# Performance work log

Measured on AMD Instinct MI355X. Metric: run time of the kernel, lower is better.

The kernel has to match this reference:

```python
import jax, jax.numpy as jnp
import numpy as np

EPS = 1e-5
K = 20


def _bn(x, gamma, beta):
    # BatchNorm in training mode: stats over all axes except last (channel)
    axes = tuple(range(x.ndim - 1))
    m = jnp.mean(x, axes, keepdims=True)
    v = jnp.var(x, axes, keepdims=True)
    return gamma * (x - m) * jax.lax.rsqrt(v + EPS) + beta


def _leaky(x):
    return jax.nn.leaky_relu(x, 0.2)


def _edge_conv(x, W, gamma, beta):
    # x: [B, N, C] channel-last. Faithful to source: topk on cdist with
    # torch default largest=True (k FARTHEST points). Squared distance
    # preserves the ordering of euclidean distance.
    sq = jnp.sum(x * x, axis=-1)                                    # [B,N]
    d2 = sq[:, :, None] + sq[:, None, :] - 2.0 * jnp.einsum('bnc,bmc->bnm', x, x)
    idx = jax.lax.top_k(d2, K)[1]                                   # [B,N,K]
    nbr = jax.vmap(lambda xi, ii: xi[ii])(x, idx)                   # [B,N,K,C]
    ctr = jnp.broadcast_to(x[:, :, None, :], nbr.shape)
    feat = jnp.concatenate([nbr - ctr, ctr], axis=-1)               # [B,N,K,2C]
    h = jnp.einsum('bnkc,oc->bnko', feat, W)                        # 1x1 conv
    return jnp.max(_leaky(_bn(h, gamma, beta)), axis=2)             # [B,N,O]


def _plane(x, w1, g1, b1, w2, g2, b2, w3, g3, b3, w4, g4, b4,
           w5, g5, b5, wl1, g6, b6, wl2, bl2, g7, b7):
    xt = jnp.transpose(x, (0, 2, 1))                                # [B,N,3]
    h1 = _edge_conv(xt, w1, g1, b1)                                 # [B,N,64]
    h2 = _edge_conv(h1, w2, g2, b2)                                 # [B,N,64]
    h3 = _edge_conv(h2, w3, g3, b3)                                 # [B,N,128]
    h4 = _edge_conv(h3, w4, g4, b4)                                 # [B,N,256]
    hc = jnp.concatenate([h1, h2, h3, h4], axis=-1)                 # [B,N,512]
    h = _leaky(_bn(jnp.einsum('bnc,oc->bno', hc, w5), g5, b5))      # [B,N,1024]
    pooled = jnp.concatenate([jnp.max(h, axis=1), jnp.mean(h, axis=1)], axis=-1)  # [B,2048]
    h = _leaky(_bn(pooled @ wl1.T, g6, b6))                         # [B,512]
    h = _leaky(_bn(h @ wl2.T + bl2, g7, b7))                        # [B,256]
    return h  # dropout p=0.0 -> identity


def setup_inputs() -> dict:
    key = jax.random.key(0)
    ks = jax.random.split(key, 16)
    B, N = 8, 2048
    f32 = jnp.float32
    d = {
        'x0': jax.random.normal(ks[0], (B, 3, N), f32),
        'x1': jax.random.normal(ks[1], (B, 3, N), f32),
        'x2': jax.random.normal(ks[2], (B, 3, N), f32),
        'w1': jax.random.normal(ks[3], (64, 6), f32) * 0.3,
        'w2': jax.random.normal(ks[4], (64, 128), f32) * 0.08,
        'w3': jax.random.normal(ks[5], (128, 128), f32) * 0.08,
        'w4': jax.random.normal(ks[6], (256, 256), f32) * 0.06,
        'w5': jax.random.normal(ks[7], (1024, 512), f32) * 0.04,
        'wl1': jax.random.normal(ks[8], (512, 2048), f32) * 0.02,
        'wl2': jax.random.normal(ks[9], (256, 512), f32) * 0.04,
        'bl2': jnp.zeros((256,), f32),
        'whead': jax.random.normal(ks[10], (7, 768), f32) * 0.03,
        'bhead': jnp.zeros((7,), f32),
    }
    for name, c in [('1', 64), ('2', 64), ('3', 128), ('4', 256), ('5', 1024),
                    ('6', 512), ('7', 256), ('8', 7)]:
        d['g' + name] = jnp.ones((c,), f32)
        d['b' + name] = jnp.zeros((c,), f32)
    return d


def reference(x0, x1, x2, w1, g1, b1, w2, g2, b2, w3, g3, b3, w4, g4, b4,
              w5, g5, b5, wl1, g6, b6, wl2, bl2, g7, b7, whead, bhead, g8, b8):
    feats = [
        _plane(x, w1, g1, b1, w2, g2, b2, w3, g3, b3, w4, g4, b4,
               w5, g5, b5, wl1, g6, b6, wl2, bl2, g7, b7)
        for x in (x0, x1, x2)
    ]
    h = jnp.concatenate(feats, axis=-1)                             # [B,768]
    # final MLP head: 1x1 conv on [B,768,1] + BN1d + ReLU + squeeze
    out = jnp.einsum('bc,oc->bo', h, whead) + bhead                 # [B,7]
    out = jax.nn.relu(_bn(out, g8, b8))
    return out
```

## Files before the change

kernel.cpp:

```cpp
#include <hip/hip_runtime.h>
#include <hip/hip_bf16.h>
#include <cstdint>
#include <cstddef>

constexpr int NB = 8;
constexpr int NP = 2048;
constexpr int BN = NB * NP;
constexpr int KK = 20;
constexpr float EPSBN = 1e-5f;
constexpr float NEG = -3.402823466e38f;
constexpr int SLOTS = 8;
constexpr int SLOTSM = 32;
constexpr int SLOTSW = 8;

typedef __attribute__((ext_vector_type(8))) short bf16x8;
typedef __attribute__((ext_vector_type(16))) float f32x16;

__device__ __forceinline__ float leaky(float x) { return x > 0.f ? x : 0.2f * x; }

__device__ __forceinline__ void split2(float x, unsigned short& h, unsigned short& l) {
    __hip_bfloat16 hh = __float2bfloat16(x);
    float hf = __bfloat162float(hh);
    __hip_bfloat16 ll = __float2bfloat16(x - hf);
    h = *reinterpret_cast<unsigned short*>(&hh);
    l = *reinterpret_cast<unsigned short*>(&ll);
}

__device__ __forceinline__ float b2f(unsigned short u) {
    __hip_bfloat16 h = *reinterpret_cast<__hip_bfloat16*>(&u);
    return __bfloat162float(h);
}

__device__ __forceinline__ unsigned int f2key(float f) {
    unsigned int u = __float_as_uint(f);
    return u ^ (unsigned int)(((int)u >> 31) | 0x80000000);
}

__global__ void k_transpose(const float* __restrict__ x, float* __restrict__ xt) {
    int i = blockIdx.x * 256 + threadIdx.x;
    if (i >= BN) return;
    int b = i >> 11, n = i & 2047;
    float4 v;
    v.x = x[(b * 3 + 0) * NP + n];
    v.y = x[(b * 3 + 1) * NP + n];
    v.z = x[(b * 3 + 2) * NP + n];
    v.w = 0.f;
    *(float4*)&xt[(size_t)i * 4] = v;
}

template <int CP4>
__global__ void k_sq4(const float4* __restrict__ FT4, float* __restrict__ sq) {
    int i = blockIdx.x * 256 + threadIdx.x;
    if (i >= BN) return;
    float s = 0.f;
#pragma unroll
    for (int cq = 0; cq < CP4; ++cq) {
        float4 f = FT4[(size_t)cq * BN + i];
        s += f.x * f.x + f.y * f.y + f.z * f.z + f.w * f.w;
    }
    sq[i] = s;
}

template <int CP>
__launch_bounds__(512, 4)
__global__ void k_knn2(const float4* __restrict__ FT4, const float* __restrict__ sq,
                       int* __restrict__ gidx) {
    constexpr int R = 8;
    constexpr int CP4 = CP / 4;
    __shared__ unsigned int ds[R][NP];
    int t = threadIdx.x;
    int b = blockIdx.x >> 8;
    int n0 = (blockIdx.x & 255) * R;
    const float4* FTb = FT4 + (size_t)b * NP;
    const float* sqb = sq + (size_t)b * NP;

    float acc[R][4];
#pragma unroll
    for (int r = 0; r < R; ++r)
#pragma unroll
        for (int mi = 0; mi < 4; ++mi) acc[r][mi] = 0.f;

    for (int cq = 0; cq < CP4; ++cq) {
        float4 f[4];
#pragma unroll
        for (int mi = 0; mi < 4; ++mi)
            f[mi] = FTb[(size_t)cq * BN + t + mi * 512];
#pragma unroll
        for (int r = 0; r < R; ++r) {
            float4 cv = FTb[(size_t)cq * BN + n0 + r];
#pragma unroll
            for (int mi = 0; mi < 4; ++mi)
                acc[r][mi] += f[mi].x * cv.x + f[mi].y * cv.y + f[mi].z * cv.z + f[mi].w * cv.w;
        }
    }
#pragma unroll
    for (int mi = 0; mi < 4; ++mi) {
        int m = t + mi * 512;
        float sm = sqb[m];
#pragma unroll
        for (int r = 0; r < R; ++r) ds[r][m] = f2key(sm - 2.f * acc[r][mi]);
    }
    __syncthreads();

    int wave = t >> 6, lane = t & 63;
    unsigned long long below = (1ull << lane) - 1ull;
    {
        int r = wave;
        unsigned int kv[32];
#pragma unroll
        for (int j = 0; j < 32; ++j) kv[j] = ds[r][lane + 64 * j];

        unsigned int T = 0;
#pragma unroll 1
        for (int bit = 31; bit >= 0; --bit) {
            unsigned int tt = T | (1u << bit);
            int c = 0;
#pragma unroll
            for (int j = 0; j < 32; ++j)
                c += (int)__popcll(__ballot(kv[j] >= tt));
            if (c >= KK) T = tt;
        }

        int obase = (b * NP + n0 + r) * KK;
        int base = 0;
#pragma unroll 1
        for (int j = 0; j < 32; ++j) {
            bool pg = kv[j] > T;
            unsigned long long mk = __ballot(pg);
            if (pg) gidx[obase + base + (int)__popcll(mk & below)] = lane + 64 * j;
            base += (int)__popcll(mk);
        }
        int rem = KK - base;
#pragma unroll 1
        for (int j = 0; j < 32; ++j) {
            if (rem <= 0) break;
            bool pe = kv[j] == T;
            unsigned long long mk = __ballot(pe);
            int myp = (int)__popcll(mk & below);
            if (pe && myp < rem) gidx[obase + base + myp] = lane + 64 * j;
            int cnt = (int)__popcll(mk);
            int take = cnt < rem ? cnt : rem;
            base += take; rem -= take;
        }
    }
}

__global__ void k_prepw(const float* __restrict__ W, int O, int Cact, int CP,
                        float* __restrict__ WaT, float* __restrict__ WdT) {
    int i = blockIdx.x * 256 + threadIdx.x;
    if (i >= CP * O) return;
    int c = i / O, o = i % O;
    float wa = (c < Cact) ? W[o * 2 * Cact + c] : 0.f;
    float wb = (c < Cact) ? W[o * 2 * Cact + Cact + c] : 0.f;
    WaT[i] = wa;
    WdT[i] = wb - wa;
}

__global__ void k_prepws2(const float* __restrict__ W, int O, int C,
                          unsigned short* __restrict__ WcH, unsigned short* __restrict__ WcL) {
    int i = blockIdx.x * 256 + threadIdx.x;
    if (i >= 2 * O * C) return;
    int r = i / C, k = i % C;
    float v;
    if (r < O) v = W[r * 2 * C + k];
    else {
        int o = r - O;
        v = W[o * 2 * C + C + k] - W[o * 2 * C + k];
    }
    split2(v, WcH[i], WcL[i]);
}

__global__ void k_splitw5(const float* __restrict__ w5, unsigned short* __restrict__ w5H,
                          unsigned short* __restrict__ w5L) {
    int i = blockIdx.x * 256 + threadIdx.x;
    if (i >= 1024 * 512) return;
    split2(w5[i], w5H[i], w5L[i]);
}

template <int O, int CP>
__launch_bounds__(O)
__global__ void k_conv(const float* __restrict__ F, int ld, const int* __restrict__ gidx,
                       const float* __restrict__ WaT, const float* __restrict__ WdT,
                       float* __restrict__ hmax, float* __restrict__ s1p,
                       float* __restrict__ s2p) {
    constexpr int CP4 = CP / 4;
    __shared__ float nbrT[2][CP][32];
    __shared__ float sctr[2][CP];
    __shared__ int sidx[2][KK];
    int t = threadIdx.x;
    int p0 = blockIdx.x * 2;
    int b = p0 >> 11;
    const float* Fb = F + (size_t)b * NP * ld;

    if (t < 2 * KK) {
        int pt = t / KK, k = t % KK;
        sidx[pt][k] = gidx[(size_t)(p0 + pt) * KK + k];
    }
    for (int e = t; e < 2 * CP; e += O) {
        int pt = e / CP, cc = e % CP;
        int n = (p0 + pt) & 2047;
        sctr[pt][cc] = Fb[(size_t)n * ld + cc];
    }
    __syncthreads();
    for (int e = t; e < 2 * KK * CP4; e += O) {
        int pt = e / (KK * CP4);
        int e2 = e % (KK * CP4);
        int k = e2 / CP4, cq = e2 % CP4;
        float4 f = *(const float4*)&Fb[(size_t)sidx[pt][k] * ld + cq * 4];
        int kp = (k + 4 * (cq & 7)) & 31;
        nbrT[pt][cq * 4 + 0][kp] = f.x;
        nbrT[pt][cq * 4 + 1][kp] = f.y;
        nbrT[pt][cq * 4 + 2][kp] = f.z;
        nbrT[pt][cq * 4 + 3][kp] = f.w;
    }
    __syncthreads();

    int o = t;
    float bacc0 = 0.f, bacc1 = 0.f;
#pragma unroll 4
    for (int c = 0; c < CP; ++c) {
        float w = WdT[c * O + o];
        bacc0 += sctr[0][c] * w;
        bacc1 += sctr[1][c] * w;
    }
    float a0[KK], a1[KK];
#pragma unroll
    for (int k = 0; k < KK; ++k) { a0[k] = 0.f; a1[k] = 0.f; }
#pragma unroll 2
    for (int c = 0; c < CP; ++c) {
        float w = WaT[c * O + o];
        int s = 4 * ((c >> 2) & 7);
#pragma unroll
        for (int kq = 0; kq < KK / 4; ++kq) {
            int kp = (4 * kq + s) & 31;
            float4 f0 = *(const float4*)&nbrT[0][c][kp];
            float4 f1 = *(const float4*)&nbrT[1][c][kp];
            a0[kq * 4 + 0] += w * f0.x; a1[kq * 4 + 0] += w * f1.x;
            a0[kq * 4 + 1] += w * f0.y; a1[kq * 4 + 1] += w * f1.y;
            a0[kq * 4 + 2] += w * f0.z; a1[kq * 4 + 2] += w * f1.z;
            a0[kq * 4 + 3] += w * f0.w; a1[kq * 4 + 3] += w * f1.w;
        }
    }
    float hm0 = NEG, hm1 = NEG, ts1 = 0.f, ts2 = 0.f;
#pragma unroll
    for (int k = 0; k < KK; ++k) {
        float h0 = a0[k] + bacc0;
        float h1 = a1[k] + bacc1;
        hm0 = fmaxf(hm0, h0); hm1 = fmaxf(hm1, h1);
        ts1 += h0 + h1; ts2 += h0 * h0 + h1 * h1;
    }
    hmax[(size_t)p0 * O + o] = hm0;
    hmax[(size_t)(p0 + 1) * O + o] = hm1;
    int slot = blockIdx.x & (SLOTS - 1);
    atomicAdd(&s1p[slot * O + o], ts1);
    atomicAdd(&s2p[slot * O + o], ts2);
}

template <int O, int C, int COFF>
__launch_bounds__(256, 4)
__global__ void k_gemms(const unsigned short* __restrict__ hcH,
                        const unsigned short* __restrict__ hcL,
                        const unsigned short* __restrict__ WdH,
                        const unsigned short* __restrict__ WdL,
                        float* __restrict__ bacc) {
    constexpr int KS = C / 16;
    int tid = threadIdx.x, wave = tid >> 6, lane = tid & 63;
    int row = lane & 31, half = lane >> 5;
    int p0 = blockIdx.x * 128 + wave * 32;
    int ob = blockIdx.y * 64;
    const unsigned short* aH = hcH + (size_t)(p0 + row) * 512 + COFF;
    const unsigned short* aL = hcL + (size_t)(p0 + row) * 512 + COFF;
    f32x16 acc[2];
#pragma unroll
    for (int nt = 0; nt < 2; ++nt)
#pragma unroll
        for (int r = 0; r < 16; ++r) acc[nt][r] = 0.f;

#pragma unroll 2
    for (int ks = 0; ks < KS; ++ks) {
        int k0 = ks * 16 + half * 8;
        bf16x8 avh = *(const bf16x8*)(aH + k0);
        bf16x8 avl = *(const bf16x8*)(aL + k0);
#pragma unroll
        for (int nt = 0; nt < 2; ++nt) {
            int j = ob + nt * 32 + row;
            bf16x8 bvh = *(const bf16x8*)(WdH + (size_t)j * C + k0);
            bf16x8 bvl = *(const bf16x8*)(WdL + (size_t)j * C + k0);
            acc[nt] = __builtin_amdgcn_mfma_f32_32x32x16_bf16(avh, bvh, acc[nt], 0, 0, 0);
            acc[nt] = __builtin_amdgcn_mfma_f32_32x32x16_bf16(avh, bvl, acc[nt], 0, 0, 0);
            acc[nt] = __builtin_amdgcn_mfma_f32_32x32x16_bf16(avl, bvh, acc[nt], 0, 0, 0);
        }
    }
#pragma unroll
    for (int nt = 0; nt < 2; ++nt)
#pragma unroll
        for (int r = 0; r < 16; ++r) {
            int i = (r & 3) + 8 * (r >> 2) + 4 * half;
            bacc[(size_t)(p0 + i) * O + ob + nt * 32 + row] = acc[nt][r];
        }
}

template <int O>
__launch_bounds__(256)
__global__ void k_gmax(const float* __restrict__ Gz, const int* __restrict__ gidx,
                       float* __restrict__ hmax, float* __restrict__ s1p,
                       float* __restrict__ s2p) {
    constexpr int PB = 256 / O;
    constexpr int O2 = 2 * O;
    __shared__ int sidx[PB][KK];
    int t = threadIdx.x;
    int pt = t / O, o = t % O;
    int p0 = blockIdx.x * PB;
    if (t < PB * KK) sidx[t / KK][t % KK] = gidx[(size_t)(p0 + t / KK) * KK + t % KK];
    __syncthreads();

    int p = p0 + pt;
    int b = p >> 11;
    const float* Gb = Gz + (size_t)b * 2048 * O2;
    float bacc = Gz[(size_t)p * O2 + O + o];
    float mx = NEG, ts1 = 0.f, ts2 = 0.f;
#pragma unroll 5
    for (int k = 0; k < KK; ++k) {
        float g = Gb[(size_t)sidx[pt][k] * O2 + o];
        float h = g + bacc;
        mx = fmaxf(mx, g);
        ts1 += h; ts2 += h * h;
    }
    hmax[(size_t)p * O + o] = mx + bacc;
    int slot = blockIdx.x & (SLOTSM - 1);
    atomicAdd(&s1p[slot * O + o], ts1);
    atomicAdd(&s2p[slot * O + o], ts2);
}

__global__ void k_redslots(const float* __restrict__ s1p, const float* __restrict__ s2p,
                           int O, int S, float* __restrict__ s1g, float* __restrict__ s2g) {
    int o = blockIdx.x * 256 + threadIdx.x;
    if (o >= O) return;
    float a = 0.f, c = 0.f;
    for (int s = 0; s < S; ++s) { a += s1p[s * O + o]; c += s2p[s * O + o]; }
    s1g[o] = a; s2g[o] = c;
}

__global__ void k_bnmax(const float* __restrict__ hmax, int O, const float* __restrict__ s1g,
                        const float* __restrict__ s2g, const float* __restrict__ gam,
                        const float* __restrict__ bet, unsigned short* __restrict__ outH,
                        unsigned short* __restrict__ outL, int ostride, int ooff,
                        float inv_cnt) {
    int i = blockIdx.x * 256 + threadIdx.x;
    if (i >= BN * O) return;
    int o = i % O, p = i / O;
    float m = s1g[o] * inv_cnt;
    float v = s2g[o] * inv_cnt - m * m;
    float rs = rsqrtf(v + EPSBN);
    float y = leaky(gam[o] * (hmax[i] - m) * rs + bet[o]);
    size_t oi = (size_t)p * ostride + ooff + o;
    split2(y, outH[oi], outL[oi]);
}

__global__ void k_pack4(const unsigned short* __restrict__ inH,
                        const unsigned short* __restrict__ inL, int coff,
                        float4* __restrict__ out) {
    __shared__ float tile[64][65];
    int tx = threadIdx.x & 63, ty = threadIdx.x >> 6;
    int p0 = blockIdx.x * 64, o0 = blockIdx.y * 64;
    for (int i = ty; i < 64; i += 4) {
        size_t idx = (size_t)(p0 + i) * 512 + coff + o0 + tx;
        tile[i][tx] = b2f(inH[idx]) + b2f(inL[idx]);
    }
    __syncthreads();
    for (int q = ty; q < 16; q += 4) {
        float4 v;
        v.x = tile[tx][4 * q + 0];
        v.y = tile[tx][4 * q + 1];
        v.z = tile[tx][4 * q + 2];
        v.w = tile[tx][4 * q + 3];
        out[(size_t)(o0 / 4 + q) * BN + p0 + tx] = v;
    }
}

__launch_bounds__(256, 3)
__global__ void k_w5ms(const unsigned short* __restrict__ hcH,
                       const unsigned short* __restrict__ hcL,
                       const unsigned short* __restrict__ w5H,
                       const unsigned short* __restrict__ w5L,
                       float* __restrict__ g5, float* __restrict__ s1p,
                       float* __restrict__ s2p) {
    int tid = threadIdx.x, wave = tid >> 6, lane = tid & 63;
    int row = lane & 31, half = lane >> 5;
    int p0 = blockIdx.x * 32;
    int ob = blockIdx.y * 512 + wave * 128;
    const unsigned short* aH = hcH + (size_t)(p0 + row) * 512;
    const unsigned short* aL = hcL + (size_t)(p0 + row) * 512;
    f32x16 acc[4];
#pragma unroll
    for (int nt = 0; nt < 4; ++nt)
#pragma unroll
        for (int r = 0; r < 16; ++r) acc[nt][r] = 0.f;

#pragma unroll 2
    for (int ks = 0; ks < 32; ++ks) {
        int k0 = ks * 16 + half * 8;
        bf16x8 avh = *(const bf16x8*)(aH + k0);
        bf16x8 avl = *(const bf16x8*)(aL + k0);
#pragma unroll
        for (int nt = 0; nt < 4; ++nt) {
            int j = ob + nt * 32 + row;
            bf16x8 bvh = *(const bf16x8*)(w5H + (size_t)j * 512 + k0);
            bf16x8 bvl = *(const bf16x8*)(w5L + (size_t)j * 512 + k0);
            acc[nt] = __builtin_amdgcn_mfma_f32_32x32x16_bf16(avh, bvh, acc[nt], 0, 0, 0);
            acc[nt] = __builtin_amdgcn_mfma_f32_32x32x16_bf16(avh, bvl, acc[nt], 0, 0, 0);
            acc[nt] = __builtin_amdgcn_mfma_f32_32x32x16_bf16(avl, bvh, acc[nt], 0, 0, 0);
        }
    }
    int slot = blockIdx.x & (SLOTSW - 1);
#pragma unroll
    for (int nt = 0; nt < 4; ++nt) {
        int j = ob + nt * 32 + row;
        float s1 = 0.f, s2 = 0.f;
#pragma unroll
        for (int r = 0; r < 16; ++r) {
            int i = (r & 3) + 8 * (r >> 2) + 4 * half;
            float v = acc[nt][r];
            g5[(size_t)(p0 + i) * 1024 + j] = v;
            s1 += v; s2 += v * v;
        }
        s1 += __shfl_xor(s1, 32);
        s2 += __shfl_xor(s2, 32);
        if (half == 0) {
            atomicAdd(&s1p[slot * 1024 + j], s1);
            atomicAdd(&s2p[slot * 1024 + j], s2);
        }
    }
}

__global__ void k_pool(const float* __restrict__ gbuf, const float* __restrict__ s1g,
                       const float* __restrict__ s2g, const float* __restrict__ gam,
                       const float* __restrict__ bet, float* __restrict__ pmax,
                       float* __restrict__ psum) {
    int t = threadIdx.x;
    int blk = blockIdx.x;
    int nc = blk & 7, ot = (blk >> 3) & 3, b = blk >> 5;
    int o = ot * 256 + t;
    float m = s1g[o] * (1.f / 16384.f);
    float v = s2g[o] * (1.f / 16384.f) - m * m;
    float rs = rsqrtf(v + EPSBN);
    float ga = gam[o], be = bet[o];
    float vmax = NEG, vsum = 0.f;
    for (int j = 0; j < 256; ++j) {
        int n = nc * 256 + j;
        float x = gbuf[((size_t)b * NP + n) * 1024 + o];
        float y = leaky(ga * (x - m) * rs + be);
        vmax = fmaxf(vmax, y);
        vsum += y;
    }
    pmax[(b * 1024 + o) * 8 + nc] = vmax;
    psum[(b * 1024 + o) * 8 + nc] = vsum;
}

__global__ void k_poolfin(const float* __restrict__ pmax, const float* __restrict__ psum,
                          float* __restrict__ pooled) {
    int i = blockIdx.x * 256 + threadIdx.x;
    if (i >= 8192) return;
    float mx = NEG, sm = 0.f;
    for (int j = 0; j < 8; ++j) {
        mx = fmaxf(mx, pmax[i * 8 + j]);
        sm += psum[i * 8 + j];
    }
    int b = i >> 10, o = i & 1023;
    pooled[b * 2048 + o] = mx;
    pooled[b * 2048 + 1024 + o] = sm * (1.f / 2048.f);
}

template <int CIN>
__global__ void k_fc(const float* __restrict__ in, const float* __restrict__ W,
                     const float* __restrict__ bias, int O, float* __restrict__ z) {
    int i = blockIdx.x * 256 + threadIdx.x;
    if (i >= NB * O) return;
    int b = i / O, o = i % O;
    const float* wr = W + (size_t)o * CIN;
    const float* ir = in + (size_t)b * CIN;
    float acc = 0.f;
#pragma unroll 4
    for (int cq = 0; cq < CIN / 4; ++cq) {
        float4 wv = *(const float4*)&wr[cq * 4];
        float4 iv = *(const float4*)&ir[cq * 4];
        acc += wv.x * iv.x + wv.y * iv.y + wv.z * iv.z + wv.w * iv.w;
    }
    z[i] = acc + (bias ? bias[o] : 0.f);
}

__global__ void k_bnb(const float* __restrict__ z, int O, const float* __restrict__ gam,
                      const float* __restrict__ bet, float* __restrict__ out, int ostride,
                      int ooff) {
    int o = blockIdx.x * 256 + threadIdx.x;
    if (o >= O) return;
    float s1 = 0.f, s2 = 0.f;
#pragma unroll
    for (int b = 0; b < NB; ++b) {
        float x = z[b * O + o];
        s1 += x; s2 += x * x;
    }
    float m = s1 * 0.125f, v = s2 * 0.125f - m * m;
    float rs = rsqrtf(v + EPSBN);
    float ga = gam[o], be = bet[o];
    for (int b = 0; b < NB; ++b) {
        float y = ga * (z[b * O + o] - m) * rs + be;
        out[b * ostride + ooff + o] = leaky(y);
    }
}

__global__ void k_head(const float* __restrict__ hf, const float* __restrict__ wh,
                       const float* __restrict__ bh, const float* __restrict__ g8,
                       const float* __restrict__ b8, float* __restrict__ out) {
    __shared__ float zh[56];
    int t = threadIdx.x;
    if (t < 56) {
        int b = t / 7, o = t % 7;
        float acc = bh[o];
        for (int c = 0; c < 768; ++c) acc += hf[b * 768 + c] * wh[o * 768 + c];
        zh[t] = acc;
    }
    __syncthreads();
    if (t < 7) {
        float s1 = 0.f, s2 = 0.f;
        for (int b = 0; b < NB; ++b) {
            float x = zh[b * 7 + t];
            s1 += x; s2 += x * x;
        }
        float m = s1 * 0.125f, v = s2 * 0.125f - m * m;
        float rs = rsqrtf(v + EPSBN);
        for (int b = 0; b < NB; ++b) {
            float y = g8[t] * (zh[b * 7 + t] - m) * rs + b8[t];
            out[b * 7 + t] = fmaxf(y, 0.f);
        }
    }
}

extern "C" void kernel_launch(void* const* d_in, const int* in_sizes, int n_in, void* d_out,
                              int out_size, void* d_ws, size_t ws_size, hipStream_t stream) {
    const float* x[3] = {(const float*)d_in[0], (const float*)d_in[1], (const float*)d_in[2]};
    const float* w1 = (const float*)d_in[3];
    const float* w2 = (const float*)d_in[4];
    const float* w3 = (const float*)d_in[5];
    const float* w4 = (const float*)d_in[6];
    const float* w5 = (const float*)d_in[7];
    const float* wl1 = (const float*)d_in[8];
    const float* wl2 = (const float*)d_in[9];
    const float* bl2 = (const float*)d_in[10];
    const float* whead = (const float*)d_in[11];
    const float* bhead = (const float*)d_in[12];
    const float *g1 = (const float*)d_in[13], *b1 = (const float*)d_in[14];
    const float *g2 = (const float*)d_in[15], *b2 = (const float*)d_in[16];
    const float *g3 = (const float*)d_in[17], *b3 = (const float*)d_in[18];
    const float *g4 = (const float*)d_in[19], *b4 = (const float*)d_in[20];
    const float *g5 = (const float*)d_in[21], *b5 = (const float*)d_in[22];
    const float *g6 = (const float*)d_in[23], *b6 = (const float*)d_in[24];
    const float *g7 = (const float*)d_in[25], *b7 = (const float*)d_in[26];
    const float *g8 = (const float*)d_in[27], *b8 = (const float*)d_in[28];

    char* w = (char*)d_ws;
    auto alloc = [&](size_t bytes) {
        char* p = w;
        w += (bytes + 255) & ~(size_t)255;
        return p;
    };
    float* xt   = (float*)alloc((size_t)BN * 4 * 4);
    unsigned short* hcH = (unsigned short*)alloc((size_t)BN * 512 * 2);
    unsigned short* hcL = (unsigned short*)alloc((size_t)BN * 512 * 2);
    float4* ft4 = (float4*)alloc((size_t)32 * BN * 16);
    float* gbig = (float*)alloc((size_t)BN * 1024 * 4);
    int*   idx  = (int*)alloc((size_t)BN * KK * 4);
    float* sqv  = (float*)alloc((size_t)BN * 4);
    float* s1g  = (float*)alloc(1024 * 4);
    float* s2g  = (float*)alloc(1024 * 4);
    float* spart  = (float*)alloc(2 * SLOTS * 256 * 4);
    float* spartC = (float*)alloc(2 * SLOTSM * 256 * 4);
    float* spartW = (float*)alloc(2 * SLOTSW * 1024 * 4);
    float* pmax = (float*)alloc(8 * 1024 * 8 * 4);
    float* psum = (float*)alloc(8 * 1024 * 8 * 4);
    float* pooled = (float*)alloc(8 * 2048 * 4);
    float* z1 = (float*)alloc(8 * 512 * 4);
    float* a1 = (float*)alloc(8 * 512 * 4);
    float* z2 = (float*)alloc(8 * 256 * 4);
    float* hfeat = (float*)alloc(8 * 768 * 4);
    float* Wa1 = (float*)alloc(4 * 64 * 4);
    float* Wd1 = (float*)alloc(4 * 64 * 4);
    unsigned short* WcH2 = (unsigned short*)alloc(128 * 64 * 2);
    unsigned short* WcL2 = (unsigned short*)alloc(128 * 64 * 2);
    unsigned short* WcH3 = (unsigned short*)alloc(256 * 64 * 2);
    unsigned short* WcL3 = (unsigned short*)alloc(256 * 64 * 2);
    unsigned short* WcH4 = (unsigned short*)alloc(512 * 128 * 2);
    unsigned short* WcL4 = (unsigned short*)alloc(512 * 128 * 2);
    unsigned short* w5H  = (unsigned short*)alloc(1024 * 512 * 2);
    unsigned short* w5L  = (unsigned short*)alloc(1024 * 512 * 2);
    float* s1p = spart;
    float* s2p = spart + SLOTS * 256;
    float* s1pc = spartC;
    float* s2pc = spartC + SLOTSM * 256;
    float* s1pw = spartW;
    float* s2pw = spartW + SLOTSW * 1024;
    float* hmaxP = gbig + (size_t)BN * 512;

    k_prepw<<<(4 * 64 + 255) / 256, 256, 0, stream>>>(w1, 64, 3, 4, Wa1, Wd1);
    k_prepws2<<<(128 * 64 + 255) / 256, 256, 0, stream>>>(w2, 64, 64, WcH2, WcL2);
    k_prepws2<<<(256 * 64 + 255) / 256, 256, 0, stream>>>(w3, 128, 64, WcH3, WcL3);
    k_prepws2<<<(512 * 128 + 255) / 256, 256, 0, stream>>>(w4, 256, 128, WcH4, WcL4);
    k_splitw5<<<(1024 * 512) / 256, 256, 0, stream>>>(w5, w5H, w5L);

    const float inv_e = 1.f / (float)(BN * KK);
    for (int p = 0; p < 3; ++p) {
        k_transpose<<<BN / 256, 256, 0, stream>>>(x[p], xt);

        k_sq4<1><<<BN / 256, 256, 0, stream>>>((const float4*)xt, sqv);
        k_knn2<4><<<NB * (NP / 8), 512, 0, stream>>>((const float4*)xt, sqv, idx);
        hipMemsetAsync(spart, 0, 2 * SLOTS * 256 * 4, stream);
        k_conv<64, 4><<<BN / 2, 64, 0, stream>>>(xt, 4, idx, Wa1, Wd1, hmaxP, s1p, s2p);
        k_redslots<<<1, 256, 0, stream>>>(s1p, s2p, 64, SLOTS, s1g, s2g);
        k_bnmax<<<(BN * 64) / 256, 256, 0, stream>>>(hmaxP, 64, s1g, s2g, g1, b1, hcH, hcL, 512, 0, inv_e);
        k_pack4<<<dim3(BN / 64, 1), 256, 0, stream>>>(hcH, hcL, 0, ft4);

        k_sq4<16><<<BN / 256, 256, 0, stream>>>(ft4, sqv);
        k_knn2<64><<<NB * (NP / 8), 512, 0, stream>>>(ft4, sqv, idx);
        k_gemms<128, 64, 0><<<dim3(BN / 128, 2), 256, 0, stream>>>(hcH, hcL, WcH2, WcL2, gbig);
        hipMemsetAsync(spartC, 0, 2 * SLOTSM * 256 * 4, stream);
        k_gmax<64><<<BN / 4, 256, 0, stream>>>(gbig, idx, hmaxP, s1pc, s2pc);
        k_redslots<<<1, 256, 0, stream>>>(s1pc, s2pc, 64, SLOTSM, s1g, s2g);
        k_bnmax<<<(BN * 64) / 256, 256, 0, stream>>>(hmaxP, 64, s1g, s2g, g2, b2, hcH, hcL, 512, 64, inv_e);
        k_pack4<<<dim3(BN / 64, 1), 256, 0, stream>>>(hcH, hcL, 64, ft4);

        k_sq4<16><<<BN / 256, 256, 0, stream>>>(ft4, sqv);
        k_knn2<64><<<NB * (NP / 8), 512, 0, stream>>>(ft4, sqv, idx);
        k_gemms<256, 64, 64><<<dim3(BN / 128, 4), 256, 0, stream>>>(hcH, hcL, WcH3, WcL3, gbig);
        hipMemsetAsync(spartC, 0, 2 * SLOTSM * 256 * 4, stream);
        k_gmax<128><<<BN / 2, 256, 0, stream>>>(gbig, idx, hmaxP, s1pc, s2pc);
        k_redslots<<<1, 256, 0, stream>>>(s1pc, s2pc, 128, SLOTSM, s1g, s2g);
        k_bnmax<<<(BN * 128) / 256, 256, 0, stream>>>(hmaxP, 128, s1g, s2g, g3, b3, hcH, hcL, 512, 128, inv_e);
        k_pack4<<<dim3(BN / 64, 2), 256, 0, stream>>>(hcH, hcL, 128, ft4);

        k_sq4<32><<<BN / 256, 256, 0, stream>>>(ft4, sqv);
        k_knn2<128><<<NB * (NP / 8), 512, 0, stream>>>(ft4, sqv, idx);
        k_gemms<512, 128, 128><<<dim3(BN / 128, 8), 256, 0, stream>>>(hcH, hcL, WcH4, WcL4, gbig);
        hipMemsetAsync(spartC, 0, 2 * SLOTSM * 256 * 4, stream);
        k_gmax<256><<<BN, 256, 0, stream>>>(gbig, idx, hmaxP, s1pc, s2pc);
        k_redslots<<<1, 256, 0, stream>>>(s1pc, s2pc, 256, SLOTSM, s1g, s2g);
        k_bnmax<<<(BN * 256) / 256, 256, 0, stream>>>(hmaxP, 256, s1g, s2g, g4, b4, hcH, hcL, 512, 256, inv_e);

        hipMemsetAsync(spartW, 0, 2 * SLOTSW * 1024 * 4, stream);
        k_w5ms<<<dim3(BN / 32, 2), 256, 0, stream>>>(hcH, hcL, w5H, w5L, gbig, s1pw, s2pw);
        k_redslots<<<4, 256, 0, stream>>>(s1pw, s2pw, 1024, SLOTSW, s1g, s2g);
        k_pool<<<256, 256, 0, stream>>>(gbig, s1g, s2g, g5, b5, pmax, psum);
        k_poolfin<<<32, 256, 0, stream>>>(pmax, psum, pooled);

        k_fc<2048><<<(8 * 512 + 255) / 256, 256, 0, stream>>>(pooled, wl1, nullptr, 512, z1);
        k_bnb<<<2, 256, 0, stream>>>(z1, 512, g6, b6, a1, 512, 0);
        k_fc<512><<<(8 * 256 + 255) / 256, 256, 0, stream>>>(a1, wl2, bl2, 256, z2);
        k_bnb<<<1, 256, 0, stream>>>(z2, 256, g7, b7, hfeat, 768, p * 256);
    }
    k_head<<<1, 64, 0, stream>>>(hfeat, whead, bhead, g8, b8, (float*)d_out);
}
```

Baseline: 3.276 ms.

## Split kNN top-k across two column halves and merge candidates

The kNN kernel now handles half of the candidate points per block, which doubles the grid and halves the per-thread accumulators and key registers. It also raises the launch-bounds occupancy hint and halves shared memory per block. Each half writes its top-20 keys and indices to scratch, and a new merge kernel picks the final 20 of the 40 candidates per point, breaking ties by lower index. The aim is more parallelism and occupancy in the distance and radix-select phase. The cost is recomputing the query loads in both halves, an extra launch, and global scratch traffic.

```diff
diff --git a/kernel.cpp b/kernel.cpp
--- a/kernel.cpp
+++ b/kernel.cpp
@@ -62,43 +62,45 @@
 }
 
 template <int CP>
-__launch_bounds__(512, 4)
-__global__ void k_knn2(const float4* __restrict__ FT4, const float* __restrict__ sq,
-                       int* __restrict__ gidx) {
+__launch_bounds__(512, 8)
+__global__ void k_knn3(const float4* __restrict__ FT4, const float* __restrict__ sq,
+                       unsigned int* __restrict__ ckey, int* __restrict__ cidx) {
     constexpr int R = 8;
     constexpr int CP4 = CP / 4;
-    __shared__ unsigned int ds[R][NP];
+    constexpr int HM = 1024;
+    __shared__ unsigned int ds[R][HM];
     int t = threadIdx.x;
-    int b = blockIdx.x >> 8;
-    int n0 = (blockIdx.x & 255) * R;
+    int bx = blockIdx.x;
+    int b = bx >> 9;
+    int rest = bx & 511;
+    int half = rest & 1;
+    int n0 = (rest >> 1) * R;
+    int mbase = half * HM;
     const float4* FTb = FT4 + (size_t)b * NP;
     const float* sqb = sq + (size_t)b * NP;
 
-    float acc[R][4];
-#pragma unroll
-    for (int r = 0; r < R; ++r)
-#pragma unroll
-        for (int mi = 0; mi < 4; ++mi) acc[r][mi] = 0.f;
+    float acc[R][2];
+#pragma unroll
+    for (int r = 0; r < R; ++r) { acc[r][0] = 0.f; acc[r][1] = 0.f; }
 
     for (int cq = 0; cq < CP4; ++cq) {
-        float4 f[4];
-#pragma unroll
-        for (int mi = 0; mi < 4; ++mi)
-            f[mi] = FTb[(size_t)cq * BN + t + mi * 512];
+        float4 f0 = FTb[(size_t)cq * BN + mbase + t];
+        float4 f1 = FTb[(size_t)cq * BN + mbase + t + 512];
 #pragma unroll
         for (int r = 0; r < R; ++r) {
             float4 cv = FTb[(size_t)cq * BN + n0 + r];
-#pragma unroll
-            for (int mi = 0; mi < 4; ++mi)
-                acc[r][mi] += f[mi].x * cv.x + f[mi].y * cv.y + f[mi].z * cv.z + f[mi].w * cv.w;
-        }
-    }
-#pragma unroll
-    for (int mi = 0; mi < 4; ++mi) {
-        int m = t + mi * 512;
-        float sm = sqb[m];
-#pragma unroll
-        for (int r = 0; r < R; ++r) ds[r][m] = f2key(sm - 2.f * acc[r][mi]);
+            acc[r][0] += f0.x * cv.x + f0.y * cv.y + f0.z * cv.z + f0.w * cv.w;
+            acc[r][1] += f1.x * cv.x + f1.y * cv.y + f1.z * cv.z + f1.w * cv.w;
+        }
+    }
+    {
+        float sm0 = sqb[mbase + t];
+        float sm1 = sqb[mbase + t + 512];
+#pragma unroll
+        for (int r = 0; r < R; ++r) {
+            ds[r][t] = f2key(sm0 - 2.f * acc[r][0]);
+            ds[r][t + 512] = f2key(sm1 - 2.f * acc[r][1]);
+        }
     }
     __syncthreads();
 
@@ -106,9 +108,9 @@
     unsigned long long below = (1ull << lane) - 1ull;
     {
         int r = wave;
-        unsigned int kv[32];
-#pragma unroll
-        for (int j = 0; j < 32; ++j) kv[j] = ds[r][lane + 64 * j];
+        unsigned int kv[16];
+#pragma unroll
+        for (int j = 0; j < 16; ++j) kv[j] = ds[r][lane + 64 * j];
 
         unsigned int T = 0;
 #pragma unroll 1
@@ -116,32 +118,64 @@
             unsigned int tt = T | (1u << bit);
             int c = 0;
 #pragma unroll
-            for (int j = 0; j < 32; ++j)
+            for (int j = 0; j < 16; ++j)
                 c += (int)__popcll(__ballot(kv[j] >= tt));
             if (c >= KK) T = tt;
         }
 
-        int obase = (b * NP + n0 + r) * KK;
+        int cb = ((b * NP + n0 + r) * 2 + half) * KK;
         int base = 0;
 #pragma unroll 1
-        for (int j = 0; j < 32; ++j) {
+        for (int j = 0; j < 16; ++j) {
             bool pg = kv[j] > T;
             unsigned long long mk = __ballot(pg);
-            if (pg) gidx[obase + base + (int)__popcll(mk & below)] = lane + 64 * j;
+            if (pg) {
+                int pos = base + (int)__popcll(mk & below);
+                ckey[cb + pos] = kv[j];
+                cidx[cb + pos] = mbase + lane + 64 * j;
+            }
             base += (int)__popcll(mk);
         }
         int rem = KK - base;
 #pragma unroll 1
-        for (int j = 0; j < 32; ++j) {
+        for (int j = 0; j < 16; ++j) {
             if (rem <= 0) break;
             bool pe = kv[j] == T;
             unsigned long long mk = __ballot(pe);
             int myp = (int)__popcll(mk & below);
-            if (pe && myp < rem) gidx[obase + base + myp] = lane + 64 * j;
+            if (pe && myp < rem) {
+                ckey[cb + base + myp] = kv[j];
+                cidx[cb + base + myp] = mbase + lane + 64 * j;
+            }
             int cnt = (int)__popcll(mk);
             int take = cnt < rem ? cnt : rem;
             base += take; rem -= take;
         }
+    }
+}
+
+__global__ void k_kmerge(const unsigned int* __restrict__ ckey, const int* __restrict__ cidx,
+                         int* __restrict__ gidx) {
+    int p = blockIdx.x * 256 + threadIdx.x;
+    if (p >= BN) return;
+    unsigned long long pk[40];
+#pragma unroll
+    for (int j = 0; j < 40; ++j) {
+        unsigned long long k = ckey[(size_t)p * 40 + j];
+        int gi = cidx[(size_t)p * 40 + j];
+        pk[j] = (k << 32) | (unsigned int)(2047 - gi);
+    }
+    unsigned long long used = 0;
+#pragma unroll 1
+    for (int it = 0; it < KK; ++it) {
+        unsigned long long bv = 0; int bj = 0;
+#pragma unroll
+        for (int j = 0; j < 40; ++j) {
+            unsigned long long v = ((used >> j) & 1ull) ? 0ull : pk[j];
+            if (v > bv) { bv = v; bj = j; }
+        }
+        used |= 1ull << bj;
+        gidx[(size_t)p * KK + it] = 2047 - (int)(bv & 0xffffffffu);
     }
 }
 
@@ -570,6 +604,8 @@
     float4* ft4 = (float4*)alloc((size_t)32 * BN * 16);
     float* gbig = (float*)alloc((size_t)BN * 1024 * 4);
     int*   idx  = (int*)alloc((size_t)BN * KK * 4);
+    unsigned int* ckey = (unsigned int*)alloc((size_t)BN * 2 * KK * 4);
+    int*   cidx = (int*)alloc((size_t)BN * 2 * KK * 4);
     float* sqv  = (float*)alloc((size_t)BN * 4);
     float* s1g  = (float*)alloc(1024 * 4);
     float* s2g  = (float*)alloc(1024 * 4);
@@ -612,7 +648,8 @@
         k_transpose<<<BN / 256, 256, 0, stream>>>(x[p], xt);
 
         k_sq4<1><<<BN / 256, 256, 0, stream>>>((const float4*)xt, sqv);
-        k_knn2<4><<<NB * (NP / 8), 512, 0, stream>>>((const float4*)xt, sqv, idx);
+        k_knn3<4><<<NB * (NP / 8) * 2, 512, 0, stream>>>((const float4*)xt, sqv, ckey, cidx);
+        k_kmerge<<<BN / 256, 256, 0, stream>>>(ckey, cidx, idx);
         hipMemsetAsync(spart, 0, 2 * SLOTS * 256 * 4, stream);
         k_conv<64, 4><<<BN / 2, 64, 0, stream>>>(xt, 4, idx, Wa1, Wd1, hmaxP, s1p, s2p);
         k_redslots<<<1, 256, 0, stream>>>(s1p, s2p, 64, SLOTS, s1g, s2g);
@@ -620,7 +657,8 @@
         k_pack4<<<dim3(BN / 64, 1), 256, 0, stream>>>(hcH, hcL, 0, ft4);
 
         k_sq4<16><<<BN / 256, 256, 0, stream>>>(ft4, sqv);
-        k_knn2<64><<<NB * (NP / 8), 512, 0, stream>>>(ft4, sqv, idx);
+        k_knn3<64><<<NB * (NP / 8) * 2, 512, 0, stream>>>(ft4, sqv, ckey, cidx);
+        k_kmerge<<<BN / 256, 256, 0, stream>>>(ckey, cidx, idx);
         k_gemms<128, 64, 0><<<dim3(BN / 128, 2), 256, 0, stream>>>(hcH, hcL, WcH2, WcL2, gbig);
         hipMemsetAsync(spartC, 0, 2 * SLOTSM * 256 * 4, stream);
         k_gmax<64><<<BN / 4, 256, 0, stream>>>(gbig, idx, hmaxP, s1pc, s2pc);
@@ -629,7 +667,8 @@
         k_pack4<<<dim3(BN / 64, 1), 256, 0, stream>>>(hcH, hcL, 64, ft4);
 
         k_sq4<16><<<BN / 256, 256, 0, stream>>>(ft4, sqv);
-        k_knn2<64><<<NB * (NP / 8), 512, 0, stream>>>(ft4, sqv, idx);
+        k_knn3<64><<<NB * (NP / 8) * 2, 512, 0, stream>>>(ft4, sqv, ckey, cidx);
+        k_kmerge<<<BN / 256, 256, 0, stream>>>(ckey, cidx, idx);
         k_gemms<256, 64, 64><<<dim3(BN / 128, 4), 256, 0, stream>>>(hcH, hcL, WcH3, WcL3, gbig);
         hipMemsetAsync(spartC, 0, 2 * SLOTSM * 256 * 4, stream);
         k_gmax<128><<<BN / 2, 256, 0, stream>>>(gbig, idx, hmaxP, s1pc, s2pc);
@@ -638,7 +677,8 @@
         k_pack4<<<dim3(BN / 64, 2), 256, 0, stream>>>(hcH, hcL, 128, ft4);
 
         k_sq4<32><<<BN / 256, 256, 0, stream>>>(ft4, sqv);
-        k_knn2<128><<<NB * (NP / 8), 512, 0, stream>>>(ft4, sqv, idx);
+        k_knn3<128><<<NB * (NP / 8) * 2, 512, 0, stream>>>(ft4, sqv, ckey, cidx);
+        k_kmerge<<<BN / 256, 256, 0, stream>>>(ckey, cidx, idx);
         k_gemms<512, 128, 128><<<dim3(BN / 128, 8), 256, 0, stream>>>(hcH, hcL, WcH4, WcL4, gbig);
         hipMemsetAsync(spartC, 0, 2 * SLOTSM * 256 * 4, stream);
         k_gmax<256><<<BN, 256, 0, stream>>>(gbig, idx, hmaxP, s1pc, s2pc);
```

Result: slower. 3.353 ms (+2.4%).
